# Optimization experiments

Measured on AMD Instinct MI355X. Metric: run time of the kernel, lower is better.

Reference implementation:

```python
import jax, jax.numpy as jnp
import numpy as np

F_DIM = 512
N_HEADS = 8
D_Q = 64
D_V = 64
EPS = 1e-6


def _xavier(key, shape):
    fan_in, fan_out = shape[0], shape[1]
    limit = float(np.sqrt(6.0 / (fan_in + fan_out)))
    return jax.random.uniform(key, shape, jnp.float32, -limit, limit)


def layer_norm(x, g, b):
    mu = jnp.mean(x, axis=-1, keepdims=True)
    var = jnp.mean(jnp.square(x - mu), axis=-1, keepdims=True)
    return (x - mu) * jax.lax.rsqrt(var + EPS) * g + b


def setup_inputs() -> dict:
    key = jax.random.key(0)
    ks = jax.random.split(key, 16)
    B, V, F = 4, 2048, F_DIM
    inp = {
        "texture_map1": jax.random.normal(ks[0], (B, V, F), jnp.float32),
        "texture_map2": jax.random.normal(ks[1], (B, V, F), jnp.float32),
        "ln1_g": jnp.ones((F,), jnp.float32), "ln1_b": jnp.zeros((F,), jnp.float32),
        "ln2_g": jnp.ones((F,), jnp.float32), "ln2_b": jnp.zeros((F,), jnp.float32),
        "Wq": _xavier(ks[2], (F, N_HEADS * D_Q)), "bq": jnp.zeros((N_HEADS * D_Q,), jnp.float32),
        "Wk": _xavier(ks[3], (F, N_HEADS * D_Q)), "bk": jnp.zeros((N_HEADS * D_Q,), jnp.float32),
        "Wv": _xavier(ks[4], (F, N_HEADS * D_V)), "bv": jnp.zeros((N_HEADS * D_V,), jnp.float32),
        "Wfc": _xavier(ks[5], (N_HEADS * D_V, F)), "bfc": jnp.zeros((F,), jnp.float32),
        "ff1_ln_g": jnp.ones((F,), jnp.float32), "ff1_ln_b": jnp.zeros((F,), jnp.float32),
        "ff1_W1": _xavier(ks[6], (F, F)), "ff1_b1": jnp.zeros((F,), jnp.float32),
        "ff1_W2": _xavier(ks[7], (F, F)), "ff1_b2": jnp.zeros((F,), jnp.float32),
        "ff2_ln_g": jnp.ones((F,), jnp.float32), "ff2_ln_b": jnp.zeros((F,), jnp.float32),
        "ff2_W1": _xavier(ks[8], (F, F)), "ff2_b1": jnp.zeros((F,), jnp.float32),
        "ff2_W2": _xavier(ks[9], (F, F)), "ff2_b2": jnp.zeros((F,), jnp.float32),
    }
    return inp


def _heads(x, d):
    B, V, _ = x.shape
    return x.reshape(B, V, N_HEADS, d).transpose(0, 2, 1, 3)  # [B,H,V,d]


def _ff_block(x, ln_g, ln_b, W1, b1, W2, b2):
    h = layer_norm(x, ln_g, ln_b)
    h = jax.nn.relu(h @ W1 + b1) @ W2 + b2
    return x + h


def reference(texture_map1, texture_map2, ln1_g, ln1_b, ln2_g, ln2_b,
              Wq, bq, Wk, bk, Wv, bv, Wfc, bfc,
              ff1_ln_g, ff1_ln_b, ff1_W1, ff1_b1, ff1_W2, ff1_b2,
              ff2_ln_g, ff2_ln_b, ff2_W1, ff2_b1, ff2_W2, ff2_b2):
    B, V, F = texture_map1.shape
    norm = D_Q ** 0.5
    t1n = layer_norm(texture_map1, ln1_g, ln1_b)
    t2n = layer_norm(texture_map2, ln2_g, ln2_b)
    q1 = _heads(t1n @ Wq + bq, D_Q)
    k1 = _heads(t1n @ Wk + bk, D_Q)
    v1 = _heads(t1n @ Wv + bv, D_V)
    q2 = _heads(t2n @ Wq + bq, D_Q)
    k2 = _heads(t2n @ Wk + bk, D_Q)
    v2 = _heads(t2n @ Wv + bv, D_V)
    # cross attention: 1 attends to 2, 2 attends to 1
    attn12 = jax.nn.softmax(jnp.einsum('bhqd,bhkd->bhqk', q1, k2) / norm, axis=-1)
    attn21 = jax.nn.softmax(jnp.einsum('bhqd,bhkd->bhqk', q2, k1) / norm, axis=-1)
    f12 = jnp.einsum('bhqk,bhkd->bhqd', attn12, v2).transpose(0, 2, 1, 3).reshape(B, V, -1)
    f21 = jnp.einsum('bhqk,bhkd->bhqd', attn21, v1).transpose(0, 2, 1, 3).reshape(B, V, -1)
    f12 = f12 @ Wfc + bfc
    f21 = f21 @ Wfc + bfc
    out1 = _ff_block(texture_map1 + f12, ff1_ln_g, ff1_ln_b, ff1_W1, ff1_b1, ff1_W2, ff1_b2)
    out2 = _ff_block(texture_map2 + f21, ff2_ln_g, ff2_ln_b, ff2_W1, ff2_b1, ff2_W2, ff2_b2)
    return (out1, out2)
```

## Files before the change

### kernel.cpp

```cpp
#include <hip/hip_runtime.h>
#include <stdint.h>

#define FD    512
#define SEQ   2048
#define NHALF 8192
#define NTOT  16384
#define QKVN  1536

typedef unsigned short u16;
typedef __attribute__((ext_vector_type(8))) short short8;
typedef __attribute__((ext_vector_type(4))) float f32x4;

__device__ __forceinline__ u16 f2bf(float f){
  union { float f; uint32_t i; } v; v.f = f;
  uint32_t r = v.i + 0x7FFFu + ((v.i >> 16) & 1u);
  return (u16)(r >> 16);
}

__device__ __forceinline__ void gload_lds16(const void* g, void* l){
  __builtin_amdgcn_global_load_lds((const __attribute__((address_space(1))) void*)g,
                                   (__attribute__((address_space(3))) void*)l, 16, 0, 0);
}

__device__ __forceinline__ f32x4 mfma16(short8 a, short8 b, f32x4 c){
  return __builtin_amdgcn_mfma_f32_16x16x32_bf16(a, b, c, 0, 0, 0);
}

__device__ __forceinline__ uint32_t cvtpk(float lo, float hi){
  uint32_t r; asm("v_cvt_pk_bf16_f32 %0, %1, %2" : "=v"(r) : "v"(lo), "v"(hi)); return r;
}

__device__ __forceinline__ float fexp2(float x){
  float r; asm("v_exp_f32 %0, %1" : "=v"(r) : "v"(x)); return r;
}

__global__ __launch_bounds__(256) void wconv_kernel(
    const float* __restrict__ w0, const float* __restrict__ w1,
    const float* __restrict__ w2, const float* __restrict__ w3,
    const float* __restrict__ w4, const float* __restrict__ w5,
    const float* __restrict__ w6, const float* __restrict__ w7,
    u16* __restrict__ out)
{
  int mat = blockIdx.x >> 6;
  const float* w = w0;
  switch (mat){ case 1: w=w1; break; case 2: w=w2; break; case 3: w=w3; break;
                case 4: w=w4; break; case 5: w=w5; break; case 6: w=w6; break;
                case 7: w=w7; break; default: break; }
  int tile = blockIdx.x & 63;
  int k0 = (tile >> 3) << 6, n0 = (tile & 7) << 6;

  __shared__ float lt[64][65];
  int tid = threadIdx.x;
  int tr = tid >> 4, tc = (tid & 15) << 2;
  #pragma unroll
  for (int p = 0; p < 4; p++){
    int k = p * 16 + tr;
    float4 v = *(const float4*)&w[(size_t)(k0 + k) * 512 + n0 + tc];
    lt[k][tc] = v.x; lt[k][tc + 1] = v.y; lt[k][tc + 2] = v.z; lt[k][tc + 3] = v.w;
  }
  __syncthreads();
  int n = tid >> 2, kc = (tid & 3) << 4;
  u16 buf[16];
  #pragma unroll
  for (int j = 0; j < 16; j++) buf[j] = f2bf(lt[kc + j][n]);
  u16* dst = out + ((size_t)mat << 18) + (size_t)(n0 + n) * 512 + k0 + kc;
  *(short8*)dst       = *(const short8*)(buf);
  *(short8*)(dst + 8) = *(const short8*)(buf + 8);
}

__global__ __launch_bounds__(256) void biascat_kernel(
    const float* __restrict__ bq, const float* __restrict__ bk,
    const float* __restrict__ bv, float* __restrict__ o)
{
  int i = blockIdx.x * 256 + threadIdx.x;
  if (i < 512) o[i] = bq[i];
  else if (i < 1024) o[i] = bk[i - 512];
  else o[i] = bv[i - 1024];
}

__global__ __launch_bounds__(256) void ln_kernel(
    const float* __restrict__ xa, const float* __restrict__ xb,
    const float* __restrict__ ga, const float* __restrict__ ba,
    const float* __restrict__ gb, const float* __restrict__ bb,
    u16* __restrict__ out)
{
  int row = blockIdx.x;
  const float* x; const float* g; const float* bi;
  if (row < NHALF){ x = xa + (size_t)row * FD; g = ga; bi = ba; }
  else            { x = xb + (size_t)(row - NHALF) * FD; g = gb; bi = bb; }
  int t = threadIdx.x;
  float2 v = ((const float2*)x)[t];
  __shared__ float red[8];
  float s = v.x + v.y;
  #pragma unroll
  for (int o = 32; o; o >>= 1) s += __shfl_xor(s, o, 64);
  if ((t & 63) == 0) red[t >> 6] = s;
  __syncthreads();
  float mu = (red[0] + red[1] + red[2] + red[3]) * (1.0f / 512.0f);
  float d0 = v.x - mu, d1 = v.y - mu;
  float q = d0 * d0 + d1 * d1;
  #pragma unroll
  for (int o = 32; o; o >>= 1) q += __shfl_xor(q, o, 64);
  if ((t & 63) == 0) red[4 + (t >> 6)] = q;
  __syncthreads();
  float var = (red[4] + red[5] + red[6] + red[7]) * (1.0f / 512.0f);
  float rs = rsqrtf(var + 1e-6f);
  out[(size_t)row * FD + 2 * t]     = f2bf(d0 * rs * g[2 * t]     + bi[2 * t]);
  out[(size_t)row * FD + 2 * t + 1] = f2bf(d1 * rs * g[2 * t + 1] + bi[2 * t + 1]);
}

__global__ __launch_bounds__(256) void vtr_kernel(
    const u16* __restrict__ qkv, u16* __restrict__ vt)
{
  int kc = blockIdx.x & 15;
  int s  = blockIdx.x >> 4;
  int dir = s >> 5, b = (s >> 3) & 3, h = s & 7;
  int t = threadIdx.x;
  int d = t & 63, kb = t >> 6;
  const u16* src = qkv + (size_t)(dir * NHALF + b * SEQ + kc * 128 + kb * 32) * QKVN
                       + 1024 + h * 64 + d;
  u16* dst = vt + (size_t)s * 131072 + (size_t)d * 2048 + kc * 128 + kb * 32;
  u16 buf[32];
  #pragma unroll
  for (int j = 0; j < 32; j++) buf[j] = src[(size_t)j * QKVN];
  #pragma unroll
  for (int j = 0; j < 4; j++)
    *(short8*)(dst + j * 8) = *(const short8*)(buf + j * 8);
}

template<bool RELU, bool OUT_BF16, bool HAS_RES>
__global__ __launch_bounds__(256) void gemm_bt(
    const u16* __restrict__ A,
    const u16* __restrict__ BtLo, const u16* __restrict__ BtHi,
    const float* __restrict__ biasLo, const float* __restrict__ biasHi,
    const float* __restrict__ resLo, const float* __restrict__ resHi,
    void* __restrict__ outp,
    int M, int N, int K, int halfM)
{
  __shared__ __align__(16) u16 lA[3][64 * 64];
  __shared__ __align__(16) u16 lB[3][64 * 64];
  int nwg = gridDim.x;
  int bid = (blockIdx.x & 7) * (nwg >> 3) + (blockIdx.x >> 3);
  int nTN = N >> 7;
  int bm = bid / nTN, bn = bid - bm * nTN;
  int rowBase = bm << 7, colBase = bn << 7;
  bool inLo = rowBase < halfM;
  const u16* Bt = inLo ? BtLo : BtHi;
  const float* bias = inLo ? biasLo : biasHi;
  const float* res = inLo ? resLo : resHi;
  int rowLocalBase = inLo ? rowBase : rowBase - halfM;

  int tid = threadIdx.x, wv = tid >> 6, ln = tid & 63;
  int g = ln >> 4, la = ln & 15;

  f32x4 acc[4][4];
  #pragma unroll
  for (int m = 0; m < 4; m++)
    #pragma unroll
    for (int n = 0; n < 4; n++) acc[m][n] = (f32x4){0.f, 0.f, 0.f, 0.f};

  int r   = tid >> 3;
  int sl  = (tid & 7) ^ (r & 7);
  int shalf = sl >> 2, sk8 = (sl & 3) << 3;
  const u16* gA0 = A  + (size_t)(rowBase + r + shalf * 64) * K + sk8;
  const u16* gB0 = Bt + (size_t)(colBase + r + shalf * 64) * K + sk8;
  const size_t row32 = (size_t)32 * K;

  int caA = (((wv >> 1) << 5) + (g << 3)) ^ ((la & 7) << 3);
  int caB = (((wv & 1) << 5) + (g << 3)) ^ ((la & 7) << 3);

  int arow = (wv >> 1) << 6, bcol = (wv & 1) << 6;

  #define STAGE(buf, kt) do { \
    gload_lds16(gA0 + (kt), (char*)lA[buf] + wv * 1024); \
    gload_lds16(gA0 + (kt) + row32, (char*)lA[buf] + 4096 + wv * 1024); \
    gload_lds16(gB0 + (kt), (char*)lB[buf] + wv * 1024); \
    gload_lds16(gB0 + (kt) + row32, (char*)lB[buf] + 4096 + wv * 1024); } while (0)

  int nK = K >> 5;
  STAGE(0, 0);
  STAGE(1, 32);

  for (int i = 0; i < nK; i++){
    if (i < nK - 1) asm volatile("s_waitcnt vmcnt(4)" ::: "memory");
    else            asm volatile("s_waitcnt vmcnt(0)" ::: "memory");
    __builtin_amdgcn_s_barrier();
    __builtin_amdgcn_sched_barrier(0);
    int cur = i % 3;
    if (i + 2 < nK) STAGE((i + 2) % 3, (i + 2) << 5);
    short8 af[4], bfr[4];
    #pragma unroll
    for (int m = 0; m < 4; m++)
      af[m] = *(const short8*)&lA[cur][((m << 4) + la) * 64 + caA];
    #pragma unroll
    for (int n = 0; n < 4; n++)
      bfr[n] = *(const short8*)&lB[cur][((n << 4) + la) * 64 + caB];
    #pragma unroll
    for (int m = 0; m < 4; m++)
      #pragma unroll
      for (int n = 0; n < 4; n++)
        acc[m][n] = mfma16(af[m], bfr[n], acc[m][n]);
  }
  #undef STAGE

  #pragma unroll
  for (int n = 0; n < 4; n++){
    int col = colBase + bcol + (n << 4) + la;
    float bv = bias[col];
    #pragma unroll
    for (int m = 0; m < 4; m++){
      int rowT = arow + (m << 4) + (g << 2);
      #pragma unroll
      for (int rr = 0; rr < 4; rr++){
        float v = acc[m][n][rr] + bv;
        if (RELU) v = fmaxf(v, 0.f);
        if (HAS_RES) v += res[(size_t)(rowLocalBase + rowT + rr) * N + col];
        if (OUT_BF16) ((u16*)outp)[(size_t)(rowBase + rowT + rr) * N + col] = f2bf(v);
        else ((float*)outp)[(size_t)(rowBase + rowT + rr) * N + col] = v;
      }
    }
  }
}

__global__ __launch_bounds__(512, 4) void attn_kernel(
    const u16* __restrict__ qkv, const u16* __restrict__ vt, u16* __restrict__ fb)
{
  int l = (blockIdx.x & 7) * 64 + (blockIdx.x >> 3);
  int qt = l & 7;
  int h  = (l >> 3) & 7;
  int z  = l >> 6;
  int dir = z >> 2, b = z & 3;
  int qRow0  = dir * NHALF + b * SEQ + qt * 256;
  int kvRow0 = (dir ^ 1) * NHALF + b * SEQ;
  int colQ = h * 64;

  __shared__ __align__(16) u16 lK[2][64 * 64];
  __shared__ __align__(16) u16 lVt[2][64 * 64];
  __shared__ __align__(16) u16 lP[8][32 * 64];

  int tid = threadIdx.x, wv = tid >> 6, ln = tid & 63;
  int g = ln >> 4, lo = ln & 15;

  int srow = tid >> 3;
  int soff = ((tid & 7) ^ (srow & 7)) * 8;

  const float CEXP = 0.18033688f;

  int ca0 = (g * 8) ^ ((lo & 7) << 3);
  int ca1 = (32 + g * 8) ^ ((lo & 7) << 3);
  int lo64 = lo * 64;

  int pidx[4];
  #pragma unroll
  for (int n = 0; n < 4; n++)
    pidx[n] = lo64 + ((n * 16 + g * 4) ^ ((lo & 7) << 3));
  int pra = lo64 + ca0, prb = lo64 + ca1;

  const u16* qbase  = qkv + (size_t)qRow0 * QKVN + colQ;
  const u16* vtbase = vt + (size_t)((dir ^ 1) * 32 + b * 8 + h) * 131072;

  const u16* kp0 = qkv + (size_t)(kvRow0 + srow) * QKVN + 512 + colQ + soff;
  const u16* vp0 = vtbase + (size_t)srow * 2048 + soff;

  char* dK0 = (char*)lK[0] + wv * 1024;
  char* dV0 = (char*)lVt[0] + wv * 1024;
  const u16* lKf = &lK[0][0];
  const u16* lVf = &lVt[0][0];
  u16* lPw = &lP[wv][0];

  gload_lds16(qbase + (size_t)srow * QKVN + soff,         (char*)lK[0]  + wv * 1024);
  gload_lds16(qbase + (size_t)(64 + srow) * QKVN + soff,  (char*)lK[1]  + wv * 1024);
  gload_lds16(qbase + (size_t)(128 + srow) * QKVN + soff, (char*)lVt[0] + wv * 1024);
  gload_lds16(qbase + (size_t)(192 + srow) * QKVN + soff, (char*)lVt[1] + wv * 1024);
  __syncthreads();
  const u16* qh;
  switch (wv >> 1){ case 0: qh = lK[0]; break; case 1: qh = lK[1]; break;
                    case 2: qh = lVt[0]; break; default: qh = lVt[1]; break; }
  int qr0 = (wv & 1) * 32 + lo;
  short8 qf00 = *(const short8*)&qh[qr0 * 64 + ca0];
  short8 qf01 = *(const short8*)&qh[qr0 * 64 + ca1];
  short8 qf10 = *(const short8*)&qh[(qr0 + 16) * 64 + ca0];
  short8 qf11 = *(const short8*)&qh[(qr0 + 16) * 64 + ca1];
  __syncthreads();

  gload_lds16(kp0, dK0);
  gload_lds16(vp0, dV0);
  kp0 += (size_t)64 * QKVN; vp0 += 64;
  __syncthreads();

  f32x4 acc_o0[4], acc_o1[4];
  #pragma unroll
  for (int nd = 0; nd < 4; nd++){
    acc_o0[nd] = (f32x4){0.f, 0.f, 0.f, 0.f};
    acc_o1[nd] = (f32x4){0.f, 0.f, 0.f, 0.f};
  }
  f32x4 acc_l0 = (f32x4){0.f, 0.f, 0.f, 0.f};
  f32x4 acc_l1 = (f32x4){0.f, 0.f, 0.f, 0.f};
  float m_l0, m_l1;
  const f32x4 z4 = (f32x4){0.f, 0.f, 0.f, 0.f};

  short8 ones;
  #pragma unroll
  for (int j = 0; j < 8; j++) ones[j] = (short)0x3F80;

  int cb = 0;
  for (int t = 0; t < 32; t++){
    if (t < 31){
      int nb = cb ^ 8192;
      gload_lds16(kp0, dK0 + nb);
      gload_lds16(vp0, dV0 + nb);
      kp0 += (size_t)64 * QKVN; vp0 += 64;
    }
    const u16* lk = (const u16*)((const char*)lKf + cb);
    const u16* lv = (const u16*)((const char*)lVf + cb);

    f32x4 s0[4], s1[4];
    #pragma unroll
    for (int n = 0; n < 4; n++){
      short8 kfa = *(const short8*)&lk[lo64 + n * 1024 + ca0];
      short8 kfb = *(const short8*)&lk[lo64 + n * 1024 + ca1];
      s0[n] = mfma16(kfa, qf00, z4);
      s0[n] = mfma16(kfb, qf01, s0[n]);
      s1[n] = mfma16(kfa, qf10, z4);
      s1[n] = mfma16(kfb, qf11, s1[n]);
    }

    float m00, m01;
    {
      float t0 = fmaxf(fmaxf(s0[0][0], s0[0][1]), fmaxf(s0[0][2], s0[0][3]));
      float t1 = fmaxf(fmaxf(s0[1][0], s0[1][1]), fmaxf(s0[1][2], s0[1][3]));
      float t2 = fmaxf(fmaxf(s0[2][0], s0[2][1]), fmaxf(s0[2][2], s0[2][3]));
      float t3 = fmaxf(fmaxf(s0[3][0], s0[3][1]), fmaxf(s0[3][2], s0[3][3]));
      m00 = fmaxf(fmaxf(t0, t1), fmaxf(t2, t3));
      m00 = fmaxf(m00, __shfl_xor(m00, 16, 64));
      m00 = fmaxf(m00, __shfl_xor(m00, 32, 64));
      m00 *= CEXP;
    }
    {
      float t0 = fmaxf(fmaxf(s1[0][0], s1[0][1]), fmaxf(s1[0][2], s1[0][3]));
      float t1 = fmaxf(fmaxf(s1[1][0], s1[1][1]), fmaxf(s1[1][2], s1[1][3]));
      float t2 = fmaxf(fmaxf(s1[2][0], s1[2][1]), fmaxf(s1[2][2], s1[2][3]));
      float t3 = fmaxf(fmaxf(s1[3][0], s1[3][1]), fmaxf(s1[3][2], s1[3][3]));
      m01 = fmaxf(fmaxf(t0, t1), fmaxf(t2, t3));
      m01 = fmaxf(m01, __shfl_xor(m01, 16, 64));
      m01 = fmaxf(m01, __shfl_xor(m01, 32, 64));
      m01 *= CEXP;
    }

    if (t == 0){ m_l0 = m00; m_l1 = m01; }

    #pragma unroll
    for (int n = 0; n < 4; n++){
      float p0 = fexp2(fmaf(s0[n][0], CEXP, -m_l0));
      float p1 = fexp2(fmaf(s0[n][1], CEXP, -m_l0));
      float p2 = fexp2(fmaf(s0[n][2], CEXP, -m_l0));
      float p3 = fexp2(fmaf(s0[n][3], CEXP, -m_l0));
      uint2 pk0; pk0.x = cvtpk(p0, p1); pk0.y = cvtpk(p2, p3);
      *(uint2*)&lPw[pidx[n]] = pk0;
      float q0 = fexp2(fmaf(s1[n][0], CEXP, -m_l1));
      float q1 = fexp2(fmaf(s1[n][1], CEXP, -m_l1));
      float q2 = fexp2(fmaf(s1[n][2], CEXP, -m_l1));
      float q3 = fexp2(fmaf(s1[n][3], CEXP, -m_l1));
      uint2 pk1; pk1.x = cvtpk(q0, q1); pk1.y = cvtpk(q2, q3);
      *(uint2*)&lPw[pidx[n] + 1024] = pk1;
    }

    short8 pf00 = *(const short8*)&lPw[pra];
    short8 pf01 = *(const short8*)&lPw[prb];
    short8 pf10 = *(const short8*)&lPw[pra + 1024];
    short8 pf11 = *(const short8*)&lPw[prb + 1024];
    acc_l0 = mfma16(pf00, ones, acc_l0);
    acc_l0 = mfma16(pf01, ones, acc_l0);
    acc_l1 = mfma16(pf10, ones, acc_l1);
    acc_l1 = mfma16(pf11, ones, acc_l1);
    #pragma unroll
    for (int nd = 0; nd < 4; nd++){
      short8 vfa = *(const short8*)&lv[lo64 + nd * 1024 + ca0];
      short8 vfb = *(const short8*)&lv[lo64 + nd * 1024 + ca1];
      acc_o0[nd] = mfma16(pf00, vfa, acc_o0[nd]);
      acc_o0[nd] = mfma16(pf01, vfb, acc_o0[nd]);
      acc_o1[nd] = mfma16(pf10, vfa, acc_o1[nd]);
      acc_o1[nd] = mfma16(pf11, vfb, acc_o1[nd]);
    }

    bool ok = (m00 <= m_l0 + 8.f) && (m01 <= m_l1 + 8.f);
    if (!__all(ok)){
      float mn0 = fmaxf(m_l0, m00);
      float mn1 = fmaxf(m_l1, m01);
      float a00 = fexp2(m_l0 - mn0);
      float a01 = fexp2(m_l1 - mn1);
      m_l0 = mn0; m_l1 = mn1;
      #pragma unroll
      for (int r = 0; r < 4; r++){
        float ar0 = __shfl(a00, g * 4 + r, 64);
        float ar1 = __shfl(a01, g * 4 + r, 64);
        acc_l0[r] *= ar0;
        acc_l1[r] *= ar1;
        #pragma unroll
        for (int nd = 0; nd < 4; nd++){
          acc_o0[nd][r] *= ar0;
          acc_o1[nd][r] *= ar1;
        }
      }
    }

    cb ^= 8192;
    __syncthreads();
  }

  #pragma unroll
  for (int r = 0; r < 4; r++){
    float rl0 = 1.0f / acc_l0[r];
    float rl1 = 1.0f / acc_l1[r];
    #pragma unroll
    for (int nd = 0; nd < 4; nd++){
      int row0 = qRow0 + wv * 32 + g * 4 + r;
      int d    = colQ + (nd << 4) + lo;
      fb[(size_t)row0 * FD + d]        = f2bf(acc_o0[nd][r] * rl0);
      fb[(size_t)(row0 + 16) * FD + d] = f2bf(acc_o1[nd][r] * rl1);
    }
  }
}

extern "C" void kernel_launch(void* const* d_in, const int* in_sizes, int n_in,
                              void* d_out, int out_size, void* d_ws, size_t ws_size,
                              hipStream_t stream)
{
  const float* t1   = (const float*)d_in[0];
  const float* t2   = (const float*)d_in[1];
  const float* ln1g = (const float*)d_in[2];
  const float* ln1b = (const float*)d_in[3];
  const float* ln2g = (const float*)d_in[4];
  const float* ln2b = (const float*)d_in[5];
  const float* Wq   = (const float*)d_in[6];
  const float* bq   = (const float*)d_in[7];
  const float* Wk   = (const float*)d_in[8];
  const float* bk   = (const float*)d_in[9];
  const float* Wv   = (const float*)d_in[10];
  const float* bv   = (const float*)d_in[11];
  const float* Wfc  = (const float*)d_in[12];
  const float* bfc  = (const float*)d_in[13];
  const float* f1lg = (const float*)d_in[14];
  const float* f1lb = (const float*)d_in[15];
  const float* W11  = (const float*)d_in[16];
  const float* b11  = (const float*)d_in[17];
  const float* W12  = (const float*)d_in[18];
  const float* b12  = (const float*)d_in[19];
  const float* f2lg = (const float*)d_in[20];
  const float* f2lb = (const float*)d_in[21];
  const float* W21  = (const float*)d_in[22];
  const float* b21  = (const float*)d_in[23];
  const float* W22  = (const float*)d_in[24];
  const float* b22  = (const float*)d_in[25];

  char* ws = (char*)d_ws;
  const size_t MB = 1024 * 1024;
  u16* wt     = (u16*)ws;
  u16* tln    = (u16*)(ws + 4 * MB);
  u16* qkv    = (u16*)(ws + 20 * MB);
  u16* fb     = (u16*)(ws + 68 * MB);
  float* bqkv = (float*)(ws + 84 * MB);
  u16* vtb    = tln;
  u16* xln    = tln;
  u16* hb     = qkv;
  float* out  = (float*)d_out;

  wconv_kernel<<<512, 256, 0, stream>>>(Wq, Wk, Wv, Wfc, W11, W12, W21, W22, wt);
  biascat_kernel<<<6, 256, 0, stream>>>(bq, bk, bv, bqkv);
  ln_kernel<<<NTOT, 256, 0, stream>>>(t1, t2, ln1g, ln1b, ln2g, ln2b, tln);
  gemm_bt<false, true, false><<<1536, 256, 0, stream>>>(
      tln, wt, wt, bqkv, bqkv, nullptr, nullptr, qkv, NTOT, QKVN, FD, NTOT);
  vtr_kernel<<<1024, 256, 0, stream>>>(qkv, vtb);
  attn_kernel<<<512, 512, 0, stream>>>(qkv, vtb, fb);
  gemm_bt<false, false, true><<<512, 256, 0, stream>>>(
      fb, wt + 3 * 262144, wt + 3 * 262144, bfc, bfc, t1, t2, out, NTOT, FD, FD, NHALF);
  ln_kernel<<<NTOT, 256, 0, stream>>>(out, out + (size_t)NHALF * FD, f1lg, f1lb, f2lg, f2lb, xln);
  gemm_bt<true, true, false><<<512, 256, 0, stream>>>(
      xln, wt + 4 * 262144, wt + 6 * 262144, b11, b21, nullptr, nullptr, hb, NTOT, FD, FD, NHALF);
  gemm_bt<false, false, true><<<512, 256, 0, stream>>>(
      hb, wt + 5 * 262144, wt + 7 * 262144, b12, b22, out, out + (size_t)NHALF * FD, out, NTOT, FD, FD, NHALF);
}
```

Baseline: 234.5 us.

## Double attention query tile per wave to 64 rows, halve block count

Each wave now handles 64 query rows (four 16-row groups) instead of 32, so blocks cover 512 queries and the grid drops from 512 to 256 blocks. The point is to reuse each K/V tile loaded into LDS across twice as many queries, cutting K/V load and LDS read traffic per unit of work. The QK and PV stages are interleaved in two key halves, Q fragments are loaded straight from global memory instead of staged through LDS, and the running max now starts at 0 rather than at the first tile's max. In exchange the kernel needs more registers, the occupancy hint is dropped, and only 256 blocks run, which may underfill a 256-CU device.

```diff
diff --git a/kernel.cpp b/kernel.cpp
--- a/kernel.cpp
+++ b/kernel.cpp
@@ -222,15 +222,15 @@
   }
 }
 
-__global__ __launch_bounds__(512, 4) void attn_kernel(
+__global__ __launch_bounds__(512) void attn_kernel(
     const u16* __restrict__ qkv, const u16* __restrict__ vt, u16* __restrict__ fb)
 {
-  int l = (blockIdx.x & 7) * 64 + (blockIdx.x >> 3);
-  int qt = l & 7;
-  int h  = (l >> 3) & 7;
-  int z  = l >> 6;
+  int l = (blockIdx.x & 7) * 32 + (blockIdx.x >> 3);
+  int qt = l & 3;
+  int h  = (l >> 2) & 7;
+  int z  = l >> 5;
   int dir = z >> 2, b = z & 3;
-  int qRow0  = dir * NHALF + b * SEQ + qt * 256;
+  int qRow0  = dir * NHALF + b * SEQ + qt * 512;
   int kvRow0 = (dir ^ 1) * NHALF + b * SEQ;
   int colQ = h * 64;
 
@@ -250,15 +250,20 @@
   int ca1 = (32 + g * 8) ^ ((lo & 7) << 3);
   int lo64 = lo * 64;
 
-  int pidx[4];
-  #pragma unroll
-  for (int n = 0; n < 4; n++)
-    pidx[n] = lo64 + ((n * 16 + g * 4) ^ ((lo & 7) << 3));
-  int pra = lo64 + ca0, prb = lo64 + ca1;
-
-  const u16* qbase  = qkv + (size_t)qRow0 * QKVN + colQ;
+  int pw[4][2], pr[4];
+  #pragma unroll
+  for (int rg = 0; rg < 4; rg++){
+    int rowp = (((rg & 1) << 4) + lo) * 64;
+    #pragma unroll
+    for (int nn = 0; nn < 2; nn++){
+      int slot = (((rg >> 1) << 2) + (nn << 1) + (g >> 1)) ^ (lo & 7);
+      pw[rg][nn] = rowp + slot * 8 + ((g & 1) << 2);
+    }
+    int slotr = (((rg >> 1) << 2) + g) ^ (lo & 7);
+    pr[rg] = rowp + slotr * 8;
+  }
+
   const u16* vtbase = vt + (size_t)((dir ^ 1) * 32 + b * 8 + h) * 131072;
-
   const u16* kp0 = qkv + (size_t)(kvRow0 + srow) * QKVN + 512 + colQ + soff;
   const u16* vp0 = vtbase + (size_t)srow * 2048 + soff;
 
@@ -268,35 +273,31 @@
   const u16* lVf = &lVt[0][0];
   u16* lPw = &lP[wv][0];
 
-  gload_lds16(qbase + (size_t)srow * QKVN + soff,         (char*)lK[0]  + wv * 1024);
-  gload_lds16(qbase + (size_t)(64 + srow) * QKVN + soff,  (char*)lK[1]  + wv * 1024);
-  gload_lds16(qbase + (size_t)(128 + srow) * QKVN + soff, (char*)lVt[0] + wv * 1024);
-  gload_lds16(qbase + (size_t)(192 + srow) * QKVN + soff, (char*)lVt[1] + wv * 1024);
-  __syncthreads();
-  const u16* qh;
-  switch (wv >> 1){ case 0: qh = lK[0]; break; case 1: qh = lK[1]; break;
-                    case 2: qh = lVt[0]; break; default: qh = lVt[1]; break; }
-  int qr0 = (wv & 1) * 32 + lo;
-  short8 qf00 = *(const short8*)&qh[qr0 * 64 + ca0];
-  short8 qf01 = *(const short8*)&qh[qr0 * 64 + ca1];
-  short8 qf10 = *(const short8*)&qh[(qr0 + 16) * 64 + ca0];
-  short8 qf11 = *(const short8*)&qh[(qr0 + 16) * 64 + ca1];
-  __syncthreads();
+  short8 qf[4][2];
+  {
+    const u16* qptr = qkv + (size_t)(qRow0 + wv * 64 + lo) * QKVN + colQ + g * 8;
+    #pragma unroll
+    for (int rg = 0; rg < 4; rg++){
+      qf[rg][0] = *(const short8*)(qptr + (size_t)(rg * 16) * QKVN);
+      qf[rg][1] = *(const short8*)(qptr + (size_t)(rg * 16) * QKVN + 32);
+    }
+  }
 
   gload_lds16(kp0, dK0);
   gload_lds16(vp0, dV0);
   kp0 += (size_t)64 * QKVN; vp0 += 64;
   __syncthreads();
 
-  f32x4 acc_o0[4], acc_o1[4];
-  #pragma unroll
-  for (int nd = 0; nd < 4; nd++){
-    acc_o0[nd] = (f32x4){0.f, 0.f, 0.f, 0.f};
-    acc_o1[nd] = (f32x4){0.f, 0.f, 0.f, 0.f};
-  }
-  f32x4 acc_l0 = (f32x4){0.f, 0.f, 0.f, 0.f};
-  f32x4 acc_l1 = (f32x4){0.f, 0.f, 0.f, 0.f};
-  float m_l0, m_l1;
+  f32x4 acc_o[4][4];
+  f32x4 acc_l[4];
+  float m_l[4];
+  #pragma unroll
+  for (int rg = 0; rg < 4; rg++){
+    #pragma unroll
+    for (int nd = 0; nd < 4; nd++) acc_o[rg][nd] = (f32x4){0.f, 0.f, 0.f, 0.f};
+    acc_l[rg] = (f32x4){0.f, 0.f, 0.f, 0.f};
+    m_l[rg] = 0.f;
+  }
   const f32x4 z4 = (f32x4){0.f, 0.f, 0.f, 0.f};
 
   short8 ones;
@@ -314,92 +315,69 @@
     const u16* lk = (const u16*)((const char*)lKf + cb);
     const u16* lv = (const u16*)((const char*)lVf + cb);
 
-    f32x4 s0[4], s1[4];
-    #pragma unroll
-    for (int n = 0; n < 4; n++){
-      short8 kfa = *(const short8*)&lk[lo64 + n * 1024 + ca0];
-      short8 kfb = *(const short8*)&lk[lo64 + n * 1024 + ca1];
-      s0[n] = mfma16(kfa, qf00, z4);
-      s0[n] = mfma16(kfb, qf01, s0[n]);
-      s1[n] = mfma16(kfa, qf10, z4);
-      s1[n] = mfma16(kfb, qf11, s1[n]);
-    }
-
-    float m00, m01;
-    {
-      float t0 = fmaxf(fmaxf(s0[0][0], s0[0][1]), fmaxf(s0[0][2], s0[0][3]));
-      float t1 = fmaxf(fmaxf(s0[1][0], s0[1][1]), fmaxf(s0[1][2], s0[1][3]));
-      float t2 = fmaxf(fmaxf(s0[2][0], s0[2][1]), fmaxf(s0[2][2], s0[2][3]));
-      float t3 = fmaxf(fmaxf(s0[3][0], s0[3][1]), fmaxf(s0[3][2], s0[3][3]));
-      m00 = fmaxf(fmaxf(t0, t1), fmaxf(t2, t3));
-      m00 = fmaxf(m00, __shfl_xor(m00, 16, 64));
-      m00 = fmaxf(m00, __shfl_xor(m00, 32, 64));
-      m00 *= CEXP;
-    }
-    {
-      float t0 = fmaxf(fmaxf(s1[0][0], s1[0][1]), fmaxf(s1[0][2], s1[0][3]));
-      float t1 = fmaxf(fmaxf(s1[1][0], s1[1][1]), fmaxf(s1[1][2], s1[1][3]));
-      float t2 = fmaxf(fmaxf(s1[2][0], s1[2][1]), fmaxf(s1[2][2], s1[2][3]));
-      float t3 = fmaxf(fmaxf(s1[3][0], s1[3][1]), fmaxf(s1[3][2], s1[3][3]));
-      m01 = fmaxf(fmaxf(t0, t1), fmaxf(t2, t3));
-      m01 = fmaxf(m01, __shfl_xor(m01, 16, 64));
-      m01 = fmaxf(m01, __shfl_xor(m01, 32, 64));
-      m01 *= CEXP;
-    }
-
-    if (t == 0){ m_l0 = m00; m_l1 = m01; }
-
-    #pragma unroll
-    for (int n = 0; n < 4; n++){
-      float p0 = fexp2(fmaf(s0[n][0], CEXP, -m_l0));
-      float p1 = fexp2(fmaf(s0[n][1], CEXP, -m_l0));
-      float p2 = fexp2(fmaf(s0[n][2], CEXP, -m_l0));
-      float p3 = fexp2(fmaf(s0[n][3], CEXP, -m_l0));
-      uint2 pk0; pk0.x = cvtpk(p0, p1); pk0.y = cvtpk(p2, p3);
-      *(uint2*)&lPw[pidx[n]] = pk0;
-      float q0 = fexp2(fmaf(s1[n][0], CEXP, -m_l1));
-      float q1 = fexp2(fmaf(s1[n][1], CEXP, -m_l1));
-      float q2 = fexp2(fmaf(s1[n][2], CEXP, -m_l1));
-      float q3 = fexp2(fmaf(s1[n][3], CEXP, -m_l1));
-      uint2 pk1; pk1.x = cvtpk(q0, q1); pk1.y = cvtpk(q2, q3);
-      *(uint2*)&lPw[pidx[n] + 1024] = pk1;
-    }
-
-    short8 pf00 = *(const short8*)&lPw[pra];
-    short8 pf01 = *(const short8*)&lPw[prb];
-    short8 pf10 = *(const short8*)&lPw[pra + 1024];
-    short8 pf11 = *(const short8*)&lPw[prb + 1024];
-    acc_l0 = mfma16(pf00, ones, acc_l0);
-    acc_l0 = mfma16(pf01, ones, acc_l0);
-    acc_l1 = mfma16(pf10, ones, acc_l1);
-    acc_l1 = mfma16(pf11, ones, acc_l1);
-    #pragma unroll
-    for (int nd = 0; nd < 4; nd++){
-      short8 vfa = *(const short8*)&lv[lo64 + nd * 1024 + ca0];
-      short8 vfb = *(const short8*)&lv[lo64 + nd * 1024 + ca1];
-      acc_o0[nd] = mfma16(pf00, vfa, acc_o0[nd]);
-      acc_o0[nd] = mfma16(pf01, vfb, acc_o0[nd]);
-      acc_o1[nd] = mfma16(pf10, vfa, acc_o1[nd]);
-      acc_o1[nd] = mfma16(pf11, vfb, acc_o1[nd]);
-    }
-
-    bool ok = (m00 <= m_l0 + 8.f) && (m01 <= m_l1 + 8.f);
+    float m0[4] = {-1e30f, -1e30f, -1e30f, -1e30f};
+
+    #pragma unroll
+    for (int kh = 0; kh < 2; kh++){
+      #pragma unroll
+      for (int nn = 0; nn < 2; nn++){
+        int n = kh * 2 + nn;
+        short8 kfa = *(const short8*)&lk[lo64 + n * 1024 + ca0];
+        short8 kfb = *(const short8*)&lk[lo64 + n * 1024 + ca1];
+        f32x4 s_[4];
+        #pragma unroll
+        for (int rg = 0; rg < 4; rg++){
+          s_[rg] = mfma16(kfa, qf[rg][0], z4);
+          s_[rg] = mfma16(kfb, qf[rg][1], s_[rg]);
+        }
+        #pragma unroll
+        for (int rg = 0; rg < 4; rg++){
+          float a = fmaxf(fmaxf(s_[rg][0], s_[rg][1]), fmaxf(s_[rg][2], s_[rg][3]));
+          m0[rg] = fmaxf(m0[rg], a);
+          float p0 = fexp2(fmaf(s_[rg][0], CEXP, -m_l[rg]));
+          float p1 = fexp2(fmaf(s_[rg][1], CEXP, -m_l[rg]));
+          float p2 = fexp2(fmaf(s_[rg][2], CEXP, -m_l[rg]));
+          float p3 = fexp2(fmaf(s_[rg][3], CEXP, -m_l[rg]));
+          uint2 w; w.x = cvtpk(p0, p1); w.y = cvtpk(p2, p3);
+          *(uint2*)&lPw[pw[rg][nn]] = w;
+        }
+      }
+      short8 pf[4];
+      #pragma unroll
+      for (int rg = 0; rg < 4; rg++){
+        pf[rg] = *(const short8*)&lPw[pr[rg]];
+        acc_l[rg] = mfma16(pf[rg], ones, acc_l[rg]);
+      }
+      int cav = kh ? ca1 : ca0;
+      #pragma unroll
+      for (int nd = 0; nd < 4; nd++){
+        short8 vf = *(const short8*)&lv[lo64 + nd * 1024 + cav];
+        #pragma unroll
+        for (int rg = 0; rg < 4; rg++)
+          acc_o[rg][nd] = mfma16(pf[rg], vf, acc_o[rg][nd]);
+      }
+    }
+
+    bool ok = true;
+    #pragma unroll
+    for (int rg = 0; rg < 4; rg++){
+      m0[rg] = fmaxf(m0[rg], __shfl_xor(m0[rg], 16, 64));
+      m0[rg] = fmaxf(m0[rg], __shfl_xor(m0[rg], 32, 64));
+      m0[rg] *= CEXP;
+      ok = ok && (m0[rg] <= m_l[rg] + 8.f);
+    }
     if (!__all(ok)){
-      float mn0 = fmaxf(m_l0, m00);
-      float mn1 = fmaxf(m_l1, m01);
-      float a00 = fexp2(m_l0 - mn0);
-      float a01 = fexp2(m_l1 - mn1);
-      m_l0 = mn0; m_l1 = mn1;
-      #pragma unroll
-      for (int r = 0; r < 4; r++){
-        float ar0 = __shfl(a00, g * 4 + r, 64);
-        float ar1 = __shfl(a01, g * 4 + r, 64);
-        acc_l0[r] *= ar0;
-        acc_l1[r] *= ar1;
+      #pragma unroll
+      for (int rg = 0; rg < 4; rg++){
+        float mn = fmaxf(m_l[rg], m0[rg]);
+        float a0 = fexp2(m_l[rg] - mn);
+        m_l[rg] = mn;
         #pragma unroll
-        for (int nd = 0; nd < 4; nd++){
-          acc_o0[nd][r] *= ar0;
-          acc_o1[nd][r] *= ar1;
+        for (int rr = 0; rr < 4; rr++){
+          float ar = __shfl(a0, g * 4 + rr, 64);
+          acc_l[rg][rr] *= ar;
+          #pragma unroll
+          for (int nd = 0; nd < 4; nd++) acc_o[rg][nd][rr] *= ar;
         }
       }
     }
@@ -409,15 +387,16 @@
   }
 
   #pragma unroll
-  for (int r = 0; r < 4; r++){
-    float rl0 = 1.0f / acc_l0[r];
-    float rl1 = 1.0f / acc_l1[r];
-    #pragma unroll
-    for (int nd = 0; nd < 4; nd++){
-      int row0 = qRow0 + wv * 32 + g * 4 + r;
-      int d    = colQ + (nd << 4) + lo;
-      fb[(size_t)row0 * FD + d]        = f2bf(acc_o0[nd][r] * rl0);
-      fb[(size_t)(row0 + 16) * FD + d] = f2bf(acc_o1[nd][r] * rl1);
+  for (int rg = 0; rg < 4; rg++){
+    #pragma unroll
+    for (int rr = 0; rr < 4; rr++){
+      float rl = 1.0f / acc_l[rg][rr];
+      #pragma unroll
+      for (int nd = 0; nd < 4; nd++){
+        int row = qRow0 + wv * 64 + rg * 16 + g * 4 + rr;
+        int d   = colQ + (nd << 4) + lo;
+        fb[(size_t)row * FD + d] = f2bf(acc_o[rg][nd][rr] * rl);
+      }
     }
   }
 }
@@ -471,7 +450,7 @@
   gemm_bt<false, true, false><<<1536, 256, 0, stream>>>(
       tln, wt, wt, bqkv, bqkv, nullptr, nullptr, qkv, NTOT, QKVN, FD, NTOT);
   vtr_kernel<<<1024, 256, 0, stream>>>(qkv, vtb);
-  attn_kernel<<<512, 512, 0, stream>>>(qkv, vtb, fb);
+  attn_kernel<<<256, 512, 0, stream>>>(qkv, vtb, fb);
   gemm_bt<false, false, true><<<512, 256, 0, stream>>>(
       fb, wt + 3 * 262144, wt + 3 * 262144, bfc, bfc, t1, t2, out, NTOT, FD, FD, NHALF);
   ln_kernel<<<NTOT, 256, 0, stream>>>(out, out + (size_t)NHALF * FD, f1lg, f1lb, f2lg, f2lb, xln);
```

After: 238.5 us. No clear change (+1.7%).
